# Kernel tuning notes

Hardware: AMD Instinct MI355X
Metric: run time of the kernel (lower is better)

Reference implementation:

```python
import jax, jax.numpy as jnp
import numpy as np

MIN_DISTANCE = 1.0
CONSTRAINT_WEIGHT = 0.02


def setup_inputs() -> dict:
    key = jax.random.key(0)
    pos = jax.random.normal(key, (16384, 3), dtype=jnp.float32) * 5.0
    return {"pos": pos}


def reference(pos):
    # pos: [N, 3]
    n = pos.shape[0]
    # Pairwise Euclidean distances via the gram trick (avoids [N,N,3] diff tensor)
    sq = jnp.sum(pos * pos, axis=-1)                      # [N]
    d2 = sq[:, None] + sq[None, :] - 2.0 * (pos @ pos.T)  # [N, N]
    d2 = jnp.maximum(d2, 0.0)
    eye = jnp.eye(n, dtype=bool)
    # keep sqrt away from 0 on the diagonal (masked to inf anyway)
    dist = jnp.sqrt(jnp.where(eye, 1.0, d2))
    dist = jnp.where(eye, jnp.inf, dist)                  # masked_fill(eye, inf)
    violations = jnp.maximum(MIN_DISTANCE - dist, 0.0)    # clamp(min=0)
    constraint_loss = jnp.mean(violations) * CONSTRAINT_WEIGHT
    return pos, constraint_loss
```

## Files before the change

### kernel.cpp

```cpp
#include <hip/hip_runtime.h>


constexpr int   N     = 16384;
constexpr int   BLOCK = 256;
constexpr int   GSZ   = 512;
constexpr int   IPT   = GSZ / BLOCK;
constexpr int   NG    = N / GSZ;
constexpr int   F     = 8;
constexpr int   NB    = NG * F;
constexpr int   QB    = 4;
constexpr int   NBINS = 512;
constexpr float BINW_INV = 8.0f;
constexpr int   MARGIN = 10;
constexpr int   CH    = 288;
constexpr int   NPB   = N / BLOCK;

__device__ __forceinline__ int zcell(float z) {
    int c = (int)floorf(z * BINW_INV) + NBINS / 2;
    return min(max(c, 0), NBINS - 1);
}

__global__ void prep_kernel(const float* __restrict__ pos, float* __restrict__ out,
                            unsigned int* __restrict__ histPart,
                            float* __restrict__ acc, unsigned int* __restrict__ cnt) {
    __shared__ unsigned int lh[NBINS];
    const int b = blockIdx.x, t = threadIdx.x;
    const int gt = b * BLOCK + t;
    lh[t] = 0u; lh[t + BLOCK] = 0u;
    if (gt == 0) { *acc = 0.0f; *cnt = 0u; }
    __syncthreads();
    if (gt < (N * 3) / 4) {
        reinterpret_cast<float4*>(out)[gt] = reinterpret_cast<const float4*>(pos)[gt];
    }
    const float z = pos[3 * gt + 2];
    atomicAdd(&lh[zcell(z)], 1u);
    __syncthreads();
    histPart[b * NBINS + t]         = lh[t];
    histPart[b * NBINS + t + BLOCK] = lh[t + BLOCK];
}

__global__ void scan_kernel(const unsigned int* __restrict__ histPart,
                            unsigned int* __restrict__ cursor,
                            int* __restrict__ jendArr) {
    __shared__ int sm[NBINS];
    const int t = threadIdx.x;
    int v = 0;
    for (int b = 0; b < NPB; ++b) v += (int)histPart[b * NBINS + t];
    sm[t] = v;
    __syncthreads();
    for (int off = 1; off < NBINS; off <<= 1) {
        const int a = (t >= off) ? sm[t - off] : 0;
        __syncthreads();
        sm[t] += a;
        __syncthreads();
    }
    cursor[t] = (unsigned int)(sm[t] - v);
    if (t < NG) {
        const int p = (t + 1) * GSZ - 1;
        int lo = 0, hi = NBINS - 1;
        while (lo < hi) {
            const int mid = (lo + hi) >> 1;
            if (sm[mid] >= p + 1) hi = mid; else lo = mid + 1;
        }
        const int jidx = lo + MARGIN;
        jendArr[t] = (jidx >= NBINS) ? N : sm[jidx - 1];
    }
}

__global__ void scatter_kernel(const float* __restrict__ pos,
                               unsigned int* __restrict__ cursor,
                               float4* __restrict__ jt4s) {
    const int t = blockIdx.x * blockDim.x + threadIdx.x;
    const float x = pos[3 * t], y = pos[3 * t + 1], z = pos[3 * t + 2];
    const unsigned int dst = atomicAdd(&cursor[zcell(z)], 1u);
    jt4s[dst] = make_float4(x, y, z, fmaf(x, x, fmaf(y, y, z * z)));
}

template <bool MASKED>
__device__ __forceinline__ float cols(const float4* __restrict__ jsm,
                                      int clen, int jbase, int i0,
                                      const float (&xi2)[IPT], const float (&yi2)[IPT],
                                      const float (&zi2)[IPT], const float (&sqi)[IPT]) {
    float s = 0.0f;
    for (int c = 0; c < clen; c += QB) {
        #pragma unroll
        for (int u = 0; u < QB; ++u) {
            const float4 pj = jsm[c + u];
            const int jq = jbase + c + u;
            #pragma unroll
            for (int k = 0; k < IPT; ++k) {
                float d = fmaf(xi2[k], pj.x, pj.w);
                d = fmaf(yi2[k], pj.y, d);
                d = fmaf(zi2[k], pj.z, d);
                const float d2 = fmaxf(d + sqi[k], 0.0f);
                float w = 1.0f - __builtin_amdgcn_sqrtf(d2);
                w = fmaxf(w, 0.0f);
                if (MASKED) w = (jq > i0 + k * BLOCK) ? w : 0.0f;
                s += w;
            }
        }
    }
    return s;
}

__global__ void __launch_bounds__(BLOCK)
pair_kernel(const float4* __restrict__ jt4s, const int* __restrict__ jendArr,
            float* __restrict__ out, float* __restrict__ acc,
            unsigned int* __restrict__ cnt) {
    __shared__ float4 jsm[CH + QB];
    __shared__ float wsum[BLOCK / 64];
    const int b = blockIdx.x;
    const int t = threadIdx.x;
    const int g = b >> 3, f = b & (F - 1);
    const int gstart = g * GSZ;
    const int i0 = gstart + t;

    const float4 w0 = jt4s[i0];
    const float4 w1 = jt4s[i0 + BLOCK];

    const int jend = jendArr[g];
    const int jbeg = gstart + 1;
    const int jlen = jend - jbeg;
    const int seg  = (((jlen + F - 1) / F) + QB - 1) & ~(QB - 1);
    const int j0   = jbeg + f * seg;
    const int len  = min(seg, jend - j0);

    float xi2[IPT], yi2[IPT], zi2[IPT], sqi[IPT];
    xi2[0] = -2.0f * w0.x; yi2[0] = -2.0f * w0.y; zi2[0] = -2.0f * w0.z; sqi[0] = w0.w;
    xi2[1] = -2.0f * w1.x; yi2[1] = -2.0f * w1.y; zi2[1] = -2.0f * w1.z; sqi[1] = w1.w;

    float s = 0.0f;
    for (int cs = 0; cs < len; cs += CH) {
        const int clen = min(CH, len - cs);
        if (t < clen)         jsm[t]         = jt4s[j0 + cs + t];
        if (t + BLOCK < clen) jsm[t + BLOCK] = jt4s[j0 + cs + t + BLOCK];
        if (t < QB) jsm[clen + t] = make_float4(0.0f, 0.0f, 1.0e6f, 4.0e12f);
        __syncthreads();
        if (j0 + cs < gstart + GSZ)
            s += cols<true >(jsm, clen, j0 + cs, i0, xi2, yi2, zi2, sqi);
        else
            s += cols<false>(jsm, clen, j0 + cs, i0, xi2, yi2, zi2, sqi);
        __syncthreads();
    }

    for (int off = 32; off > 0; off >>= 1) s += __shfl_down(s, off);
    if ((t & 63) == 0) wsum[t >> 6] = s;
    __syncthreads();
    if (t == 0) {
        float bs = 0.0f;
        #pragma unroll
        for (int w = 0; w < BLOCK / 64; ++w) bs += wsum[w];
        atomicAdd(acc, bs);
        __threadfence();
        const unsigned int done = atomicAdd(cnt, 1u);
        if (done == (unsigned int)(NB - 1)) {
            __threadfence();
            const float total = atomicAdd(acc, 0.0f);
            const double mean = 2.0 * (double)total / ((double)N * (double)N);
            out[(size_t)N * 3] = (float)(mean * 0.02);
        }
    }
}

extern "C" void kernel_launch(void* const* d_in, const int* in_sizes, int n_in,
                              void* d_out, int out_size, void* d_ws, size_t ws_size,
                              hipStream_t stream) {
    const float* pos = (const float*)d_in[0];
    float* out = (float*)d_out;
    float*        acc      = (float*)d_ws;
    unsigned int* cnt      = (unsigned int*)d_ws + 1;
    int*          jendArr  = (int*)((char*)d_ws + 256);
    unsigned int* cursor   = (unsigned int*)((char*)d_ws + 512);
    unsigned int* histPart = (unsigned int*)((char*)d_ws + 4096);
    float4*       jt4s     = (float4*)((char*)d_ws + 135168);

    prep_kernel   <<<NPB, BLOCK, 0, stream>>>(pos, out, histPart, acc, cnt);
    scan_kernel   <<<1, NBINS, 0, stream>>>(histPart, cursor, jendArr);
    scatter_kernel<<<NPB, BLOCK, 0, stream>>>(pos, cursor, jt4s);
    pair_kernel   <<<NB, BLOCK, 0, stream>>>(jt4s, jendArr, out, acc, cnt);
}
```

Before: 91.85 us.

## Fuse prep, scan, scatter and pair kernels into one cooperative kernel

Replaces the four-kernel pipeline with a single cooperative launch that uses grid-wide syncs between the histogram, scan/scatter and pair phases, removing three kernel launch boundaries. Each block redundantly re-sums all partial histograms and rescans, and ranks come from shared-memory atomics, so the separate cursor atomics are no longer needed. The bin count is halved and made coarser, with the margin adjusted, which changes how many candidate columns each group scans. The risks are the cost of grid.sync, the redundant per-block work over 64 histograms, and the requirement that all 256 blocks be co-resident.

```diff
diff --git a/kernel.cpp b/kernel.cpp
--- a/kernel.cpp
+++ b/kernel.cpp
@@ -1,4 +1,7 @@
 #include <hip/hip_runtime.h>
+#include <hip/hip_cooperative_groups.h>
+
+namespace cg = cooperative_groups;
 
 
 constexpr int   N     = 16384;
@@ -9,71 +12,15 @@
 constexpr int   F     = 8;
 constexpr int   NB    = NG * F;
 constexpr int   QB    = 4;
-constexpr int   NBINS = 512;
-constexpr float BINW_INV = 8.0f;
-constexpr int   MARGIN = 10;
+constexpr int   NBINS = 256;
+constexpr float BINW_INV = 4.0f;
+constexpr int   MARGIN = 6;
 constexpr int   CH    = 288;
-constexpr int   NPB   = N / BLOCK;
+constexpr int   NHB   = N / BLOCK;
 
 __device__ __forceinline__ int zcell(float z) {
     int c = (int)floorf(z * BINW_INV) + NBINS / 2;
     return min(max(c, 0), NBINS - 1);
-}
-
-__global__ void prep_kernel(const float* __restrict__ pos, float* __restrict__ out,
-                            unsigned int* __restrict__ histPart,
-                            float* __restrict__ acc, unsigned int* __restrict__ cnt) {
-    __shared__ unsigned int lh[NBINS];
-    const int b = blockIdx.x, t = threadIdx.x;
-    const int gt = b * BLOCK + t;
-    lh[t] = 0u; lh[t + BLOCK] = 0u;
-    if (gt == 0) { *acc = 0.0f; *cnt = 0u; }
-    __syncthreads();
-    if (gt < (N * 3) / 4) {
-        reinterpret_cast<float4*>(out)[gt] = reinterpret_cast<const float4*>(pos)[gt];
-    }
-    const float z = pos[3 * gt + 2];
-    atomicAdd(&lh[zcell(z)], 1u);
-    __syncthreads();
-    histPart[b * NBINS + t]         = lh[t];
-    histPart[b * NBINS + t + BLOCK] = lh[t + BLOCK];
-}
-
-__global__ void scan_kernel(const unsigned int* __restrict__ histPart,
-                            unsigned int* __restrict__ cursor,
-                            int* __restrict__ jendArr) {
-    __shared__ int sm[NBINS];
-    const int t = threadIdx.x;
-    int v = 0;
-    for (int b = 0; b < NPB; ++b) v += (int)histPart[b * NBINS + t];
-    sm[t] = v;
-    __syncthreads();
-    for (int off = 1; off < NBINS; off <<= 1) {
-        const int a = (t >= off) ? sm[t - off] : 0;
-        __syncthreads();
-        sm[t] += a;
-        __syncthreads();
-    }
-    cursor[t] = (unsigned int)(sm[t] - v);
-    if (t < NG) {
-        const int p = (t + 1) * GSZ - 1;
-        int lo = 0, hi = NBINS - 1;
-        while (lo < hi) {
-            const int mid = (lo + hi) >> 1;
-            if (sm[mid] >= p + 1) hi = mid; else lo = mid + 1;
-        }
-        const int jidx = lo + MARGIN;
-        jendArr[t] = (jidx >= NBINS) ? N : sm[jidx - 1];
-    }
-}
-
-__global__ void scatter_kernel(const float* __restrict__ pos,
-                               unsigned int* __restrict__ cursor,
-                               float4* __restrict__ jt4s) {
-    const int t = blockIdx.x * blockDim.x + threadIdx.x;
-    const float x = pos[3 * t], y = pos[3 * t + 1], z = pos[3 * t + 2];
-    const unsigned int dst = atomicAdd(&cursor[zcell(z)], 1u);
-    jt4s[dst] = make_float4(x, y, z, fmaf(x, x, fmaf(y, y, z * z)));
 }
 
 template <bool MASKED>
@@ -104,21 +51,81 @@
 }
 
 __global__ void __launch_bounds__(BLOCK)
-pair_kernel(const float4* __restrict__ jt4s, const int* __restrict__ jendArr,
-            float* __restrict__ out, float* __restrict__ acc,
-            unsigned int* __restrict__ cnt) {
+fused_kernel(const float* __restrict__ pos, float* __restrict__ out,
+             unsigned int* __restrict__ histPart, float4* __restrict__ jt4s,
+             float* __restrict__ acc, unsigned int* __restrict__ cnt) {
+    __shared__ unsigned int lh[NBINS];
+    __shared__ int sm[NBINS];
+    __shared__ int beforeB[NBINS];
     __shared__ float4 jsm[CH + QB];
     __shared__ float wsum[BLOCK / 64];
+
+    const cg::grid_group grid = cg::this_grid();
     const int b = blockIdx.x;
     const int t = threadIdx.x;
+    const int gt = b * BLOCK + t;
+
+    float px = 0.0f, py = 0.0f, pz = 0.0f;
+    int cell = 0;
+    unsigned int rank = 0u;
+    if (b < NHB) {
+        lh[t] = 0u;
+        if (gt == 0) { atomicExch(acc, 0.0f); atomicExch(cnt, 0u); }
+        __syncthreads();
+        if (gt < (N * 3) / 4) {
+            reinterpret_cast<float4*>(out)[gt] =
+                reinterpret_cast<const float4*>(pos)[gt];
+        }
+        px = pos[3 * gt]; py = pos[3 * gt + 1]; pz = pos[3 * gt + 2];
+        cell = zcell(pz);
+        rank = atomicAdd(&lh[cell], 1u);
+        __syncthreads();
+        histPart[b * NBINS + t] = lh[t];
+        __threadfence();
+    }
+    grid.sync();
+
+    {
+        int v = 0, bef = 0;
+        for (int p = 0; p < NHB; ++p) {
+            const int hv = (int)histPart[p * NBINS + t];
+            if (p == b) bef = v;
+            v += hv;
+        }
+        sm[t] = v; beforeB[t] = bef;
+    }
+    __syncthreads();
+    for (int off = 1; off < NBINS; off <<= 1) {
+        const int a = (t >= off) ? sm[t - off] : 0;
+        __syncthreads();
+        sm[t] += a;
+        __syncthreads();
+    }
+    if (b < NHB) {
+        const int ex = (cell > 0) ? sm[cell - 1] : 0;
+        const unsigned int dst = (unsigned int)(ex + beforeB[cell]) + rank;
+        jt4s[dst] = make_float4(px, py, pz, fmaf(px, px, fmaf(py, py, pz * pz)));
+        __threadfence();
+    }
     const int g = b >> 3, f = b & (F - 1);
+    int jend;
+    {
+        const int p = (g + 1) * GSZ - 1;
+        int lo = 0, hi = NBINS - 1;
+        while (lo < hi) {
+            const int mid = (lo + hi) >> 1;
+            if (sm[mid] >= p + 1) hi = mid; else lo = mid + 1;
+        }
+        const int jidx = lo + MARGIN;
+        jend = (jidx >= NBINS) ? N : sm[jidx - 1];
+    }
+    grid.sync();
+
     const int gstart = g * GSZ;
     const int i0 = gstart + t;
-
     const float4 w0 = jt4s[i0];
     const float4 w1 = jt4s[i0 + BLOCK];
 
-    const int jend = jendArr[g];
     const int jbeg = gstart + 1;
     const int jlen = jend - jbeg;
     const int seg  = (((jlen + F - 1) / F) + QB - 1) & ~(QB - 1);
@@ -134,7 +141,7 @@
         const int clen = min(CH, len - cs);
         if (t < clen)         jsm[t]         = jt4s[j0 + cs + t];
         if (t + BLOCK < clen) jsm[t + BLOCK] = jt4s[j0 + cs + t + BLOCK];
-        if (t < QB) jsm[clen + t] = make_float4(0.0f, 0.0f, 1.0e6f, 4.0e12f);
+        if (t < QB) jsm[max(clen, 0) + t] = make_float4(0.0f, 0.0f, 1.0e6f, 4.0e12f);
         __syncthreads();
         if (j0 + cs < gstart + GSZ)
             s += cols<true >(jsm, clen, j0 + cs, i0, xi2, yi2, zi2, sqi);
@@ -169,13 +176,12 @@
     float* out = (float*)d_out;
     float*        acc      = (float*)d_ws;
     unsigned int* cnt      = (unsigned int*)d_ws + 1;
-    int*          jendArr  = (int*)((char*)d_ws + 256);
-    unsigned int* cursor   = (unsigned int*)((char*)d_ws + 512);
     unsigned int* histPart = (unsigned int*)((char*)d_ws + 4096);
-    float4*       jt4s     = (float4*)((char*)d_ws + 135168);
+    float4*       jt4s     = (float4*)((char*)d_ws + 131072);
 
-    prep_kernel   <<<NPB, BLOCK, 0, stream>>>(pos, out, histPart, acc, cnt);
-    scan_kernel   <<<1, NBINS, 0, stream>>>(histPart, cursor, jendArr);
-    scatter_kernel<<<NPB, BLOCK, 0, stream>>>(pos, cursor, jt4s);
-    pair_kernel   <<<NB, BLOCK, 0, stream>>>(jt4s, jendArr, out, acc, cnt);
+    void* args[] = { (void*)&pos, (void*)&out, (void*)&histPart,
+                     (void*)&jt4s, (void*)&acc, (void*)&cnt };
+    hipLaunchCooperativeKernel((void (*)(const float*, float*, unsigned int*,
+                                         float4*, float*, unsigned int*))fused_kernel,
+                               dim3(NB), dim3(BLOCK), args, 0, stream);
 }
```

Result: slower. 151.8 us (+65.3%).

## Merge scan into scatter with redundant per-block scan and precomputed ranks

Applied to the files above, without the earlier changes.

Removes the single-block scan kernel: every scatter block now re-reads all partial histograms, performs the prefix scan itself, and computes destinations from ranks recorded in prep, with no global atomics. The z-bins are halved (256 bins, wider cells, smaller margin) so each thread owns one bin. This saves one kernel launch and the serial single-block scan, at the cost of redundant histogram reads per block. The coarser bins with a smaller margin change how far each group's j range extends, which shifts pair-kernel work.

```diff
diff --git a/kernel.cpp b/kernel.cpp
--- a/kernel.cpp
+++ b/kernel.cpp
@@ -9,44 +9,53 @@
 constexpr int   F     = 8;
 constexpr int   NB    = NG * F;
 constexpr int   QB    = 4;
-constexpr int   NBINS = 512;
-constexpr float BINW_INV = 8.0f;
-constexpr int   MARGIN = 10;
+constexpr int   NBINS = 256;
+constexpr float BINW_INV = 4.0f;
+constexpr int   MARGIN = 6;
 constexpr int   CH    = 288;
-constexpr int   NPB   = N / BLOCK;
+constexpr int   NHB   = N / BLOCK;
 
 __device__ __forceinline__ int zcell(float z) {
     int c = (int)floorf(z * BINW_INV) + NBINS / 2;
     return min(max(c, 0), NBINS - 1);
 }
 
-__global__ void prep_kernel(const float* __restrict__ pos, float* __restrict__ out,
-                            unsigned int* __restrict__ histPart,
-                            float* __restrict__ acc, unsigned int* __restrict__ cnt) {
+__global__ void __launch_bounds__(BLOCK)
+prep_kernel(const float* __restrict__ pos, float* __restrict__ out,
+            unsigned int* __restrict__ histPart, unsigned int* __restrict__ crk,
+            float* __restrict__ acc, unsigned int* __restrict__ cnt) {
     __shared__ unsigned int lh[NBINS];
     const int b = blockIdx.x, t = threadIdx.x;
     const int gt = b * BLOCK + t;
-    lh[t] = 0u; lh[t + BLOCK] = 0u;
+    lh[t] = 0u;
     if (gt == 0) { *acc = 0.0f; *cnt = 0u; }
     __syncthreads();
     if (gt < (N * 3) / 4) {
         reinterpret_cast<float4*>(out)[gt] = reinterpret_cast<const float4*>(pos)[gt];
     }
     const float z = pos[3 * gt + 2];
-    atomicAdd(&lh[zcell(z)], 1u);
+    const int cell = zcell(z);
+    const unsigned int rank = atomicAdd(&lh[cell], 1u);
+    crk[gt] = (unsigned int)cell | (rank << 16);
     __syncthreads();
-    histPart[b * NBINS + t]         = lh[t];
-    histPart[b * NBINS + t + BLOCK] = lh[t + BLOCK];
+    histPart[b * NBINS + t] = lh[t];
 }
 
-__global__ void scan_kernel(const unsigned int* __restrict__ histPart,
-                            unsigned int* __restrict__ cursor,
-                            int* __restrict__ jendArr) {
+__global__ void __launch_bounds__(BLOCK)
+scatter_kernel(const float* __restrict__ pos, const unsigned int* __restrict__ histPart,
+               const unsigned int* __restrict__ crk, float4* __restrict__ jt4s,
+               int* __restrict__ jendArr) {
     __shared__ int sm[NBINS];
-    const int t = threadIdx.x;
-    int v = 0;
-    for (int b = 0; b < NPB; ++b) v += (int)histPart[b * NBINS + t];
-    sm[t] = v;
+    __shared__ int beforeB[NBINS];
+    const int b = blockIdx.x, t = threadIdx.x;
+    int v = 0, bef = 0;
+    #pragma unroll 8
+    for (int p = 0; p < NHB; ++p) {
+        const int hv = (int)histPart[p * NBINS + t];
+        if (p == b) bef = v;
+        v += hv;
+    }
+    sm[t] = v; beforeB[t] = bef;
     __syncthreads();
     for (int off = 1; off < NBINS; off <<= 1) {
         const int a = (t >= off) ? sm[t - off] : 0;
@@ -54,8 +63,15 @@
         sm[t] += a;
         __syncthreads();
     }
-    cursor[t] = (unsigned int)(sm[t] - v);
-    if (t < NG) {
+    const int gt = b * BLOCK + t;
+    const unsigned int cr = crk[gt];
+    const int cell = (int)(cr & 0xffffu);
+    const int rank = (int)(cr >> 16);
+    const int ex   = (cell > 0) ? sm[cell - 1] : 0;
+    const int dst  = ex + beforeB[cell] + rank;
+    const float x = pos[3 * gt], y = pos[3 * gt + 1], z = pos[3 * gt + 2];
+    jt4s[dst] = make_float4(x, y, z, fmaf(x, x, fmaf(y, y, z * z)));
+    if (b == 0 && t < NG) {
         const int p = (t + 1) * GSZ - 1;
         int lo = 0, hi = NBINS - 1;
         while (lo < hi) {
@@ -65,15 +81,6 @@
         const int jidx = lo + MARGIN;
         jendArr[t] = (jidx >= NBINS) ? N : sm[jidx - 1];
     }
-}
-
-__global__ void scatter_kernel(const float* __restrict__ pos,
-                               unsigned int* __restrict__ cursor,
-                               float4* __restrict__ jt4s) {
-    const int t = blockIdx.x * blockDim.x + threadIdx.x;
-    const float x = pos[3 * t], y = pos[3 * t + 1], z = pos[3 * t + 2];
-    const unsigned int dst = atomicAdd(&cursor[zcell(z)], 1u);
-    jt4s[dst] = make_float4(x, y, z, fmaf(x, x, fmaf(y, y, z * z)));
 }
 
 template <bool MASKED>
@@ -170,12 +177,11 @@
     float*        acc      = (float*)d_ws;
     unsigned int* cnt      = (unsigned int*)d_ws + 1;
     int*          jendArr  = (int*)((char*)d_ws + 256);
-    unsigned int* cursor   = (unsigned int*)((char*)d_ws + 512);
     unsigned int* histPart = (unsigned int*)((char*)d_ws + 4096);
+    unsigned int* crk      = (unsigned int*)((char*)d_ws + 69632);
     float4*       jt4s     = (float4*)((char*)d_ws + 135168);
 
-    prep_kernel   <<<NPB, BLOCK, 0, stream>>>(pos, out, histPart, acc, cnt);
-    scan_kernel   <<<1, NBINS, 0, stream>>>(histPart, cursor, jendArr);
-    scatter_kernel<<<NPB, BLOCK, 0, stream>>>(pos, cursor, jt4s);
-    pair_kernel   <<<NB, BLOCK, 0, stream>>>(jt4s, jendArr, out, acc, cnt);
+    prep_kernel   <<<NHB, BLOCK, 0, stream>>>(pos, out, histPart, crk, acc, cnt);
+    scatter_kernel<<<NHB, BLOCK, 0, stream>>>(pos, histPart, crk, jt4s, jendArr);
+    pair_kernel   <<<NB,  BLOCK, 0, stream>>>(jt4s, jendArr, out, acc, cnt);
 }
```

New measurement: 82.00 us. -10.7%, faster.
